# Performance work log

Measured on AMD Instinct MI355X. Metric: run time of the kernel, lower is better.

Reference implementation:

```python
import jax, jax.numpy as jnp
import numpy as np
from jax import lax

B, C, OUT, K, H, W = 8, 64, 32, 3, 64, 64


def _conv2d(x, w, b, stride=1, pad=0, groups=1):
    o = lax.conv_general_dilated(x, w, (stride, stride), [(pad, pad), (pad, pad)],
                                 dimension_numbers=('NCHW', 'OIHW', 'NCHW'),
                                 feature_group_count=groups)
    return o + b[None, :, None, None]


def _bn(x, g, b, m, v, eps=1e-5):
    # eval-mode BatchNorm2d with running stats
    s = g / jnp.sqrt(v + eps)
    return x * s[None, :, None, None] + (b - m * s)[None, :, None, None]


def _eca(x, w):
    # global avg pool -> 1D conv over channel axis -> sigmoid gate [b,c,1,1]
    y = x.mean((-2, -1))[:, None, :]  # [b,1,c]
    y = lax.conv_general_dilated(y, w, (1,), [(1, 1)],
                                 dimension_numbers=('NCW', 'OIW', 'NCW'))
    return jax.nn.sigmoid(y[:, 0, :])[:, :, None, None]


def _avgpool3(x):
    # AvgPool2d(k=3, stride=1, pad=1), count_include_pad=True (torch default)
    s = lax.reduce_window(x, 0.0, lax.add, (1, 1, 3, 3), (1, 1, 1, 1),
                          [(0, 0), (0, 0), (1, 1), (1, 1)])
    return s / 9.0


def _forward(x, sc_w, sc_b, ac_w, ac_b, oc_w, oc_b, oc_bn_g, oc_bn_b, oc_bn_m, oc_bn_v,
             ex_w, ey_w, ez_w, ff_w, ff_b, g1_w, g1_b, g2_w, g2_b,
             fu_w, fu_b, fu_bn_g, fu_bn_b, fu_bn_m, fu_bn_v):
    b, c, h, w = x.shape
    k = K
    # --- ReceptiveFieldAttentionConv ---
    frf = jax.nn.silu(_conv2d(x, sc_w, sc_b, pad=k // 2, groups=c))
    frf = frf.reshape(b, c, k * k, h, w)
    arf = _conv2d(_avgpool3(x), ac_w, ac_b, groups=c).reshape(b, c, k * k, h, w)
    arf = jax.nn.softmax(arf, axis=2)  # softmax over k*k RF positions
    wt = (frf * arf).reshape(b, c, k, k, h, w)
    wt = wt.transpose(0, 1, 4, 2, 5, 3).reshape(b, c, h * k, w * k)  # pixel-shuffle-like
    x_rfa = jax.nn.silu(_bn(_conv2d(wt, oc_w, oc_b, stride=k, groups=4),
                            oc_bn_g, oc_bn_b, oc_bn_m, oc_bn_v))
    # --- FrequencyGroupedChannelAttention ---
    energy = jnp.abs(jnp.fft.fft2(x)).mean((-2, -1))  # [b,c]
    ranks = jnp.argsort(jnp.argsort(-energy, axis=1), axis=1)
    mask = (ranks < c // 2).astype(x.dtype)[:, :, None, None]  # top-half-energy channels
    a_x = _eca(x, ex_w)
    a_y = _eca(x * mask, ey_w)
    a_z = _eca(x * (1.0 - mask), ez_w)
    a_f = _conv2d(jnp.concatenate([a_y, a_z], 1), ff_w, ff_b, groups=4)
    g_in = jnp.concatenate([a_f, a_x], 1)
    g = jax.nn.sigmoid(_conv2d(jax.nn.silu(_conv2d(g_in, g1_w, g1_b)), g2_w, g2_b))
    x_fgca = x * (g * a_f + (1.0 - g) * a_x)
    # --- fuse ---
    fused = jnp.concatenate([x_rfa, x_fgca], 1)
    return jax.nn.silu(_bn(_conv2d(fused, fu_w, fu_b),
                           fu_bn_g, fu_bn_b, fu_bn_m, fu_bn_v))


def setup_inputs() -> dict:
    key = jax.random.key(0)
    ks = jax.random.split(key, 32)
    rn = lambda k, shp, s=0.1: jax.random.normal(k, shp, jnp.float32) * s
    gh = max(8, C // 4)  # gate hidden = 16
    return {
        'x': jax.random.normal(ks[0], (B, C, H, W), jnp.float32),
        'sc_w': rn(ks[1], (C * K * K, 1, K, K)), 'sc_b': rn(ks[2], (C * K * K,)),
        'ac_w': rn(ks[3], (C * K * K, 1, 1, 1)), 'ac_b': rn(ks[4], (C * K * K,)),
        'oc_w': rn(ks[5], (C, C // 4, K, K)), 'oc_b': rn(ks[6], (C,)),
        'oc_bn_g': 1.0 + rn(ks[7], (C,)), 'oc_bn_b': rn(ks[8], (C,)),
        'oc_bn_m': rn(ks[9], (C,)), 'oc_bn_v': 0.9 + 0.2 * jax.random.uniform(ks[10], (C,), jnp.float32),
        'ex_w': rn(ks[11], (1, 1, 3), 0.3), 'ey_w': rn(ks[12], (1, 1, 3), 0.3),
        'ez_w': rn(ks[13], (1, 1, 3), 0.3),
        'ff_w': rn(ks[14], (C, 2 * C // 4, 1, 1)), 'ff_b': rn(ks[15], (C,)),
        'g1_w': rn(ks[16], (gh, 2 * C, 1, 1)), 'g1_b': rn(ks[17], (gh,)),
        'g2_w': rn(ks[18], (C, gh, 1, 1)), 'g2_b': rn(ks[19], (C,)),
        'fu_w': rn(ks[20], (OUT, 2 * C, 1, 1)), 'fu_b': rn(ks[21], (OUT,)),
        'fu_bn_g': 1.0 + rn(ks[22], (OUT,)), 'fu_bn_b': rn(ks[23], (OUT,)),
        'fu_bn_m': rn(ks[24], (OUT,)), 'fu_bn_v': 0.9 + 0.2 * jax.random.uniform(ks[25], (OUT,), jnp.float32),
    }


def reference(x, sc_w, sc_b, ac_w, ac_b, oc_w, oc_b, oc_bn_g, oc_bn_b, oc_bn_m, oc_bn_v,
              ex_w, ey_w, ez_w, ff_w, ff_b, g1_w, g1_b, g2_w, g2_b,
              fu_w, fu_b, fu_bn_g, fu_bn_b, fu_bn_m, fu_bn_v):
    return _forward(x, sc_w, sc_b, ac_w, ac_b, oc_w, oc_b, oc_bn_g, oc_bn_b, oc_bn_m, oc_bn_v,
                    ex_w, ey_w, ez_w, ff_w, ff_b, g1_w, g1_b, g2_w, g2_b,
                    fu_w, fu_b, fu_bn_g, fu_bn_b, fu_bn_m, fu_bn_v)
```

## Files before the change

kernel.cpp:

```cpp
#include <hip/hip_runtime.h>
#include <math.h>

#define EPS 1e-5f

__device__ __forceinline__ float wave_sum(float v) {
  v += __shfl_down(v, 32);
  v += __shfl_down(v, 16);
  v += __shfl_down(v, 8);
  v += __shfl_down(v, 4);
  v += __shfl_down(v, 2);
  v += __shfl_down(v, 1);
  return v;
}

__device__ __forceinline__ float silu_f(float v) { return v / (1.f + __expf(-v)); }
__device__ __forceinline__ float sigm_f(float v) { return 1.f / (1.f + __expf(-v)); }

__device__ __forceinline__ int bitrev6(int v) {
  return ((v & 1) << 5) | ((v & 2) << 3) | ((v & 4) << 1) |
         ((v & 8) >> 1) | ((v & 16) >> 3) | ((v & 32) >> 5);
}

__global__ __launch_bounds__(256) void k_dft(const float* __restrict__ x,
                                             float* __restrict__ energy,
                                             float* __restrict__ meanx) {
  __shared__ float re1[64 * 65];
  __shared__ float im1[64 * 65];
  __shared__ float redA[4], redB[4];
  const int bc = blockIdx.x;
  const int tid = threadIdx.x;
  const int lane = tid & 63;
  const int wv = tid >> 6;
  const float* xp = x + (size_t)bc * 4096;

  float twc[6], tws[6];
#pragma unroll
  for (int s = 0; s < 6; ++s) {
    int half = 32 >> s;
    if (lane & half) {
      float ang = -6.283185307179586f * (float)((lane & (half - 1)) << s) / 64.f;
      float sv, cv;
      __sincosf(ang, &sv, &cv);
      twc[s] = cv;
      tws[s] = sv;
    } else {
      twc[s] = 1.f;
      tws[s] = 0.f;
    }
  }

  const int f = bitrev6(lane);
  const int fm = (64 - f) & 63;
  const int plane = bitrev6(fm);

  float lsum = 0.f;
#pragma unroll 1
  for (int rp = 0; rp < 8; ++rp) {
    const int h0 = wv * 16 + rp * 2;
    float zr = xp[h0 * 64 + lane];
    float zi = xp[(h0 + 1) * 64 + lane];
    lsum += zr + zi;
#pragma unroll
    for (int s = 0; s < 6; ++s) {
      const int half = 32 >> s;
      const bool up = (lane & half) != 0;
      float pr = __shfl_xor(zr, half);
      float pi = __shfl_xor(zi, half);
      float tr = up ? pr - zr : zr + pr;
      float ti = up ? pi - zi : zi + pi;
      const float c = twc[s], sn = tws[s];
      zr = tr * c - ti * sn;
      zi = tr * sn + ti * c;
    }
    float mr = __shfl(zr, plane);
    float mi = __shfl(zi, plane);
    float ar = 0.5f * (zr + mr), ai = 0.5f * (zi - mi);
    float br = 0.5f * (zi + mi), bi = 0.5f * (mr - zr);
    re1[f * 65 + h0] = ar;
    im1[f * 65 + h0] = ai;
    re1[f * 65 + h0 + 1] = br;
    im1[f * 65 + h0 + 1] = bi;
  }
  __syncthreads();

  float msum = 0.f;
#pragma unroll 1
  for (int i = 0; i < 9; ++i) {
    const int kv = wv + 4 * i;
    if (kv > 32) break;
    const float wgt = (kv == 0 || kv == 32) ? 1.f : 2.f;
    float ar = re1[kv * 65 + lane];
    float ai = im1[kv * 65 + lane];
#pragma unroll
    for (int s = 0; s < 6; ++s) {
      const int half = 32 >> s;
      const bool up = (lane & half) != 0;
      float pr = __shfl_xor(ar, half);
      float pi = __shfl_xor(ai, half);
      float tr = up ? pr - ar : ar + pr;
      float ti = up ? pi - ai : ai + pi;
      const float c = twc[s], sn = tws[s];
      ar = tr * c - ti * sn;
      ai = tr * sn + ti * c;
    }
    msum += wgt * sqrtf(ar * ar + ai * ai);
  }

  msum = wave_sum(msum);
  lsum = wave_sum(lsum);
  if (lane == 0) { redA[wv] = msum; redB[wv] = lsum; }
  __syncthreads();
  if (tid == 0) {
    float e = redA[0] + redA[1] + redA[2] + redA[3];
    float m = redB[0] + redB[1] + redB[2] + redB[3];
    energy[bc] = e * (1.f / 4096.f);
    meanx[bc] = m * (1.f / 4096.f);
  }
}

__global__ __launch_bounds__(64) void k_attn(
    const float* __restrict__ energy, const float* __restrict__ meanx,
    const float* __restrict__ ex_w, const float* __restrict__ ey_w,
    const float* __restrict__ ez_w, const float* __restrict__ ff_w,
    const float* __restrict__ ff_b, const float* __restrict__ g1_w,
    const float* __restrict__ g1_b, const float* __restrict__ g2_w,
    const float* __restrict__ g2_b, float* __restrict__ s2) {
  __shared__ float e[64], mx[64], my[64], mz[64];
  __shared__ float ax[64], ay[64], az[64], af[64], h1[16];
  const int b = blockIdx.x;
  const int c = threadIdx.x;
  e[c] = energy[b * 64 + c];
  mx[c] = meanx[b * 64 + c];
  __syncthreads();
  int rank = 0;
  float ec = e[c];
  for (int i = 0; i < 64; ++i) {
    float ei = e[i];
    rank += (ei > ec) || (ei == ec && i < c);
  }
  float mask = (rank < 32) ? 1.f : 0.f;
  my[c] = mx[c] * mask;
  mz[c] = mx[c] * (1.f - mask);
  __syncthreads();
  {
    float l, r, m;
    l = (c > 0) ? mx[c - 1] : 0.f; m = mx[c]; r = (c < 63) ? mx[c + 1] : 0.f;
    ax[c] = sigm_f(ex_w[0] * l + ex_w[1] * m + ex_w[2] * r);
    l = (c > 0) ? my[c - 1] : 0.f; m = my[c]; r = (c < 63) ? my[c + 1] : 0.f;
    ay[c] = sigm_f(ey_w[0] * l + ey_w[1] * m + ey_w[2] * r);
    l = (c > 0) ? mz[c - 1] : 0.f; m = mz[c]; r = (c < 63) ? mz[c + 1] : 0.f;
    az[c] = sigm_f(ez_w[0] * l + ez_w[1] * m + ez_w[2] * r);
  }
  __syncthreads();
  {
    int g = c >> 4;
    float acc = ff_b[c];
#pragma unroll
    for (int i = 0; i < 32; ++i) {
      int ch = g * 32 + i;
      float v = (ch < 64) ? ay[ch] : az[ch - 64];
      acc = fmaf(v, ff_w[c * 32 + i], acc);
    }
    af[c] = acc;
  }
  __syncthreads();
  if (c < 16) {
    float a = g1_b[c];
#pragma unroll
    for (int i = 0; i < 64; ++i) a = fmaf(af[i], g1_w[c * 128 + i], a);
#pragma unroll
    for (int i = 0; i < 64; ++i) a = fmaf(ax[i], g1_w[c * 128 + 64 + i], a);
    h1[c] = silu_f(a);
  }
  __syncthreads();
  float gv = g2_b[c];
#pragma unroll
  for (int o = 0; o < 16; ++o) gv = fmaf(h1[o], g2_w[c * 16 + o], gv);
  gv = sigm_f(gv);
  s2[b * 64 + c] = gv * af[c] + (1.f - gv) * ax[c];
}

__global__ __launch_bounds__(256) void k_rfa(
    const float* __restrict__ x,
    const float* __restrict__ sc_w, const float* __restrict__ sc_b,
    const float* __restrict__ ac_w, const float* __restrict__ ac_b,
    const float* __restrict__ oc_w, const float* __restrict__ oc_b,
    const float* __restrict__ bn_g, const float* __restrict__ bn_b,
    const float* __restrict__ bn_m, const float* __restrict__ bn_v,
    float* __restrict__ xrfa) {
  __shared__ __align__(16) float scwp[16 * 9 * 12];
  __shared__ __align__(16) float mp[16 * 24];
  __shared__ __align__(16) float ocwp[16 * 16 * 12];
  const int blk = blockIdx.x;
  const int band = blk & 7;
  const int g = (blk >> 3) & 3;
  const int b = blk >> 5;
  const int tid = threadIdx.x;
  const int lane = tid & 63;
  const int wv = tid >> 6;

  for (int i = tid; i < 1296; i += 256) {
    int icg = i / 81, rem = i - icg * 81;
    int j = rem / 9, t = rem - j * 9;
    scwp[icg * 108 + j * 12 + t] = sc_w[(g * 144 + icg * 9 + j) * 9 + t];
  }
  if (tid < 144) {
    int icg = tid / 9, j = tid - icg * 9;
    scwp[icg * 108 + j * 12 + 9] = sc_b[g * 144 + tid];
    mp[icg * 24 + j] = ac_w[g * 144 + tid];
    mp[icg * 24 + 12 + j] = ac_b[g * 144 + tid];
  }
  for (int i = tid; i < 2304; i += 256) {
    int oco = i / 144, rem = i - oco * 144;
    int icg = rem / 9, j = rem - icg * 9;
    ocwp[icg * 192 + oco * 12 + j] = oc_w[((g * 16 + oco) * 16 + icg) * 9 + j];
  }
  __syncthreads();

  const int r0 = band * 8 + wv * 2;
  const int w = lane;
  const bool vW = w > 0, vE = w < 63;
  float acc0[16], acc1[16];
#pragma unroll
  for (int i = 0; i < 16; ++i) { acc0[i] = 0.f; acc1[i] = 0.f; }

  const float* xg = x + ((size_t)(b * 64 + g * 16)) * 4096 + w;

#pragma unroll 1
  for (int icg = 0; icg < 16; ++icg) {
    const float* xc = xg + icg * 4096;
    float n[12];
#pragma unroll
    for (int t = 0; t < 4; ++t) {
      int h = r0 - 1 + t;
      bool vh = (h >= 0) && (h < 64);
      const float* row = xc + h * 64;
      n[t * 3 + 0] = (vh && vW) ? row[-1] : 0.f;
      n[t * 3 + 1] = vh ? row[0] : 0.f;
      n[t * 3 + 2] = (vh && vE) ? row[1] : 0.f;
    }
    float rs0 = n[0] + n[1] + n[2];
    float rs1 = n[3] + n[4] + n[5];
    float rs2 = n[6] + n[7] + n[8];
    float rs3 = n[9] + n[10] + n[11];
    float ap0 = (rs0 + rs1 + rs2) * (1.f / 9.f);
    float ap1 = (rs1 + rs2 + rs3) * (1.f / 9.f);

    float aw[12], ab[12];
    *(float4*)&aw[0] = *(const float4*)&mp[icg * 24];
    *(float4*)&aw[4] = *(const float4*)&mp[icg * 24 + 4];
    *(float4*)&aw[8] = *(const float4*)&mp[icg * 24 + 8];
    *(float4*)&ab[0] = *(const float4*)&mp[icg * 24 + 12];
    *(float4*)&ab[4] = *(const float4*)&mp[icg * 24 + 16];
    *(float4*)&ab[8] = *(const float4*)&mp[icg * 24 + 20];

    float f0[9], f1[9], a0[9], a1[9];
    float amax0 = -1e30f, amax1 = -1e30f;
#pragma unroll
    for (int j = 0; j < 9; ++j) {
      float wt[12];
      *(float4*)&wt[0] = *(const float4*)&scwp[icg * 108 + j * 12];
      *(float4*)&wt[4] = *(const float4*)&scwp[icg * 108 + j * 12 + 4];
      *(float4*)&wt[8] = *(const float4*)&scwp[icg * 108 + j * 12 + 8];
      float p0 = wt[9], p1 = wt[9];
#pragma unroll
      for (int t = 0; t < 9; ++t) {
        p0 = fmaf(n[t], wt[t], p0);
        p1 = fmaf(n[t + 3], wt[t], p1);
      }
      f0[j] = silu_f(p0);
      f1[j] = silu_f(p1);
      float v0 = fmaf(ap0, aw[j], ab[j]);
      float v1 = fmaf(ap1, aw[j], ab[j]);
      a0[j] = v0; a1[j] = v1;
      amax0 = fmaxf(amax0, v0);
      amax1 = fmaxf(amax1, v1);
    }
    float es0 = 0.f, es1 = 0.f;
    float p0[9], p1[9];
#pragma unroll
    for (int j = 0; j < 9; ++j) {
      float e0 = __expf(a0[j] - amax0);
      float e1 = __expf(a1[j] - amax1);
      es0 += e0; es1 += e1;
      p0[j] = f0[j] * e0;
      p1[j] = f1[j] * e1;
    }
    float i0 = __fdividef(1.f, es0);
    float i1 = __fdividef(1.f, es1);
#pragma unroll
    for (int j = 0; j < 9; ++j) { p0[j] *= i0; p1[j] *= i1; }

#pragma unroll
    for (int oco = 0; oco < 16; ++oco) {
      float ov[12];
      *(float4*)&ov[0] = *(const float4*)&ocwp[icg * 192 + oco * 12];
      *(float4*)&ov[4] = *(const float4*)&ocwp[icg * 192 + oco * 12 + 4];
      *(float4*)&ov[8] = *(const float4*)&ocwp[icg * 192 + oco * 12 + 8];
      float s0 = 0.f, s1 = 0.f;
#pragma unroll
      for (int j = 0; j < 9; ++j) {
        s0 = fmaf(p0[j], ov[j], s0);
        s1 = fmaf(p1[j], ov[j], s1);
      }
      acc0[oco] += s0;
      acc1[oco] += s1;
    }
  }

  float* op = xrfa + ((size_t)(b * 64 + g * 16)) * 4096 + r0 * 64 + w;
#pragma unroll
  for (int oco = 0; oco < 16; ++oco) {
    int oc = g * 16 + oco;
    float s = bn_g[oc] * rsqrtf(bn_v[oc] + EPS);
    float bb = bn_b[oc] - bn_m[oc] * s;
    float ob = oc_b[oc];
    float v0 = fmaf(acc0[oco] + ob, s, bb);
    float v1 = fmaf(acc1[oco] + ob, s, bb);
    op[oco * 4096] = silu_f(v0);
    op[oco * 4096 + 64] = silu_f(v1);
  }
}

__global__ __launch_bounds__(256) void k_fuse(
    const float* __restrict__ x, const float* __restrict__ xrfa,
    const float* __restrict__ s2, const float* __restrict__ fu_w,
    const float* __restrict__ fu_b, const float* __restrict__ bn_g,
    const float* __restrict__ bn_b, const float* __restrict__ bn_m,
    const float* __restrict__ bn_v, float* __restrict__ out) {
  __shared__ float red[3 * 64 * 33];
  __shared__ __align__(16) float fw[4096];
  const int blk = blockIdx.x;
  const int tid = threadIdx.x;
  const int sloc = tid & 63;
  const int chunk = __builtin_amdgcn_readfirstlane(tid >> 6);
  const int b = blk >> 6;
  const int sp = (blk & 63) * 64 + sloc;
  const int cb = (chunk & 1) * 32;
  const int wb = chunk * 32;

  for (int i = tid; i < 1024; i += 256)
    ((float4*)fw)[i] = ((const float4*)fu_w)[i];

  const float* src = (chunk < 2) ? xrfa : x;
  const float* ip = src + ((size_t)(b * 64 + cb)) * 4096 + sp;
  float inv[32];
  if (chunk < 2) {
#pragma unroll
    for (int i = 0; i < 32; ++i) inv[i] = ip[i * 4096];
  } else {
#pragma unroll
    for (int i = 0; i < 32; ++i) inv[i] = ip[i * 4096] * s2[b * 64 + cb + i];
  }
  __syncthreads();

  float acc[32];
#pragma unroll
  for (int oc = 0; oc < 32; ++oc) {
    const float* wr = &fw[oc * 128 + wb];
    float a = 0.f;
#pragma unroll
    for (int q = 0; q < 8; ++q) {
      float4 wv4 = *(const float4*)&wr[q * 4];
      a = fmaf(inv[q * 4 + 0], wv4.x, a);
      a = fmaf(inv[q * 4 + 1], wv4.y, a);
      a = fmaf(inv[q * 4 + 2], wv4.z, a);
      a = fmaf(inv[q * 4 + 3], wv4.w, a);
    }
    acc[oc] = a;
  }

  if (chunk != 0) {
    float* rp = &red[(chunk - 1) * 2112 + sloc * 33];
#pragma unroll
    for (int oc = 0; oc < 32; ++oc) rp[oc] = acc[oc];
  }
  __syncthreads();
  if (chunk == 0) {
#pragma unroll
    for (int oc = 0; oc < 32; ++oc)
      acc[oc] += red[sloc * 33 + oc] + red[2112 + sloc * 33 + oc] +
                 red[4224 + sloc * 33 + oc];
    float* op = out + ((size_t)b * 32) * 4096 + sp;
#pragma unroll
    for (int oc = 0; oc < 32; ++oc) {
      float s = bn_g[oc] * rsqrtf(bn_v[oc] + EPS);
      float v = acc[oc] + fu_b[oc];
      v = fmaf(v, s, bn_b[oc] - bn_m[oc] * s);
      op[oc * 4096] = silu_f(v);
    }
  }
}

extern "C" void kernel_launch(void* const* d_in, const int* in_sizes, int n_in,
                              void* d_out, int out_size, void* d_ws, size_t ws_size,
                              hipStream_t stream) {
  const float* x       = (const float*)d_in[0];
  const float* sc_w    = (const float*)d_in[1];
  const float* sc_b    = (const float*)d_in[2];
  const float* ac_w    = (const float*)d_in[3];
  const float* ac_b    = (const float*)d_in[4];
  const float* oc_w    = (const float*)d_in[5];
  const float* oc_b    = (const float*)d_in[6];
  const float* oc_bn_g = (const float*)d_in[7];
  const float* oc_bn_b = (const float*)d_in[8];
  const float* oc_bn_m = (const float*)d_in[9];
  const float* oc_bn_v = (const float*)d_in[10];
  const float* ex_w    = (const float*)d_in[11];
  const float* ey_w    = (const float*)d_in[12];
  const float* ez_w    = (const float*)d_in[13];
  const float* ff_w    = (const float*)d_in[14];
  const float* ff_b    = (const float*)d_in[15];
  const float* g1_w    = (const float*)d_in[16];
  const float* g1_b    = (const float*)d_in[17];
  const float* g2_w    = (const float*)d_in[18];
  const float* g2_b    = (const float*)d_in[19];
  const float* fu_w    = (const float*)d_in[20];
  const float* fu_b    = (const float*)d_in[21];
  const float* fu_bn_g = (const float*)d_in[22];
  const float* fu_bn_b = (const float*)d_in[23];
  const float* fu_bn_m = (const float*)d_in[24];
  const float* fu_bn_v = (const float*)d_in[25];

  float* ws     = (float*)d_ws;
  float* energy = ws;
  float* meanx  = ws + 512;
  float* s2     = ws + 1024;
  float* xrfa   = ws + 2048;

  k_dft<<<512, 256, 0, stream>>>(x, energy, meanx);
  k_attn<<<8, 64, 0, stream>>>(energy, meanx, ex_w, ey_w, ez_w,
                               ff_w, ff_b, g1_w, g1_b, g2_w, g2_b, s2);
  k_rfa<<<256, 256, 0, stream>>>(x, sc_w, sc_b, ac_w, ac_b, oc_w, oc_b,
                                 oc_bn_g, oc_bn_b, oc_bn_m, oc_bn_v, xrfa);
  k_fuse<<<512, 256, 0, stream>>>(x, xrfa, s2, fu_w, fu_b,
                                  fu_bn_g, fu_bn_b, fu_bn_m, fu_bn_v,
                                  (float*)d_out);
}
```

Baseline: 190.3 us.

## Batch FFT rows, split RFA channel loop across waves, reorganize fuse by output channel

Three kernels change together. The DFT kernel now handles two complex row pairs per butterfly pass, keeps only the non-redundant half spectrum (f<=32) in shared memory, and transforms two columns per iteration. The RFA conv kernel doubles its grid by splitting the 16 input channels between wave pairs and summing the partials through shared memory. The fuse kernel makes each wave load all 128 input channels and compute 8 output channels, which removes the cross-wave reduction. Together these aim to raise parallelism and ILP and cut shared-memory and reduction overhead, at the cost of higher register pressure in the fuse kernel (128 live inputs) and an extra shared-memory reduction step in RFA.

```diff
diff --git a/kernel.cpp b/kernel.cpp
--- a/kernel.cpp
+++ b/kernel.cpp
@@ -21,11 +21,26 @@
          ((v & 8) >> 1) | ((v & 16) >> 3) | ((v & 32) >> 5);
 }
 
+#define FFT6(zr, zi)                                           \
+  do {                                                         \
+    _Pragma("unroll") for (int s = 0; s < 6; ++s) {            \
+      const int half = 32 >> s;                                \
+      const bool up = (lane & half) != 0;                      \
+      float pr = __shfl_xor(zr, half);                         \
+      float pi = __shfl_xor(zi, half);                         \
+      float tr = up ? pr - zr : zr + pr;                       \
+      float ti = up ? pi - zi : zi + pi;                       \
+      const float c = twc[s], sn = tws[s];                     \
+      zr = tr * c - ti * sn;                                   \
+      zi = tr * sn + ti * c;                                   \
+    }                                                          \
+  } while (0)
+
 __global__ __launch_bounds__(256) void k_dft(const float* __restrict__ x,
                                              float* __restrict__ energy,
                                              float* __restrict__ meanx) {
-  __shared__ float re1[64 * 65];
-  __shared__ float im1[64 * 65];
+  __shared__ float re1[33 * 65];
+  __shared__ float im1[33 * 65];
   __shared__ float redA[4], redB[4];
   const int bc = blockIdx.x;
   const int tid = threadIdx.x;
@@ -55,55 +70,82 @@
 
   float lsum = 0.f;
 #pragma unroll 1
-  for (int rp = 0; rp < 8; ++rp) {
-    const int h0 = wv * 16 + rp * 2;
-    float zr = xp[h0 * 64 + lane];
-    float zi = xp[(h0 + 1) * 64 + lane];
-    lsum += zr + zi;
+  for (int rp = 0; rp < 4; ++rp) {
+    const int h0 = wv * 16 + rp * 4;
+    float x0 = xp[h0 * 64 + lane];
+    float x1 = xp[(h0 + 1) * 64 + lane];
+    float x2 = xp[(h0 + 2) * 64 + lane];
+    float x3 = xp[(h0 + 3) * 64 + lane];
+    lsum += x0 + x1 + x2 + x3;
+    float zr = x0, zi = x1, yr = x2, yi = x3;
 #pragma unroll
     for (int s = 0; s < 6; ++s) {
       const int half = 32 >> s;
       const bool up = (lane & half) != 0;
-      float pr = __shfl_xor(zr, half);
-      float pi = __shfl_xor(zi, half);
-      float tr = up ? pr - zr : zr + pr;
-      float ti = up ? pi - zi : zi + pi;
+      float pzr = __shfl_xor(zr, half);
+      float pzi = __shfl_xor(zi, half);
+      float pyr = __shfl_xor(yr, half);
+      float pyi = __shfl_xor(yi, half);
+      float tzr = up ? pzr - zr : zr + pzr;
+      float tzi = up ? pzi - zi : zi + pzi;
+      float tyr = up ? pyr - yr : yr + pyr;
+      float tyi = up ? pyi - yi : yi + pyi;
       const float c = twc[s], sn = tws[s];
-      zr = tr * c - ti * sn;
-      zi = tr * sn + ti * c;
-    }
-    float mr = __shfl(zr, plane);
-    float mi = __shfl(zi, plane);
-    float ar = 0.5f * (zr + mr), ai = 0.5f * (zi - mi);
-    float br = 0.5f * (zi + mi), bi = 0.5f * (mr - zr);
-    re1[f * 65 + h0] = ar;
-    im1[f * 65 + h0] = ai;
-    re1[f * 65 + h0 + 1] = br;
-    im1[f * 65 + h0 + 1] = bi;
+      zr = tzr * c - tzi * sn;
+      zi = tzr * sn + tzi * c;
+      yr = tyr * c - tyi * sn;
+      yi = tyr * sn + tyi * c;
+    }
+    float mzr = __shfl(zr, plane), mzi = __shfl(zi, plane);
+    float myr = __shfl(yr, plane), myi = __shfl(yi, plane);
+    if (f <= 32) {
+      float ar = 0.5f * (zr + mzr), ai = 0.5f * (zi - mzi);
+      float br = 0.5f * (zi + mzi), bi = 0.5f * (mzr - zr);
+      float cr = 0.5f * (yr + myr), ci = 0.5f * (yi - myi);
+      float dr = 0.5f * (yi + myi), di = 0.5f * (myr - yr);
+      re1[f * 65 + h0] = ar;     im1[f * 65 + h0] = ai;
+      re1[f * 65 + h0 + 1] = br; im1[f * 65 + h0 + 1] = bi;
+      re1[f * 65 + h0 + 2] = cr; im1[f * 65 + h0 + 2] = ci;
+      re1[f * 65 + h0 + 3] = dr; im1[f * 65 + h0 + 3] = di;
+    }
   }
   __syncthreads();
 
   float msum = 0.f;
 #pragma unroll 1
-  for (int i = 0; i < 9; ++i) {
-    const int kv = wv + 4 * i;
-    if (kv > 32) break;
-    const float wgt = (kv == 0 || kv == 32) ? 1.f : 2.f;
-    float ar = re1[kv * 65 + lane];
-    float ai = im1[kv * 65 + lane];
+  for (int i = 0; i < 4; ++i) {
+    const int kv1 = wv + 8 * i;
+    const int kv2 = kv1 + 4;
+    const float w1 = (kv1 == 0) ? 1.f : 2.f;
+    float ar = re1[kv1 * 65 + lane];
+    float ai = im1[kv1 * 65 + lane];
+    float br = re1[kv2 * 65 + lane];
+    float bi = im1[kv2 * 65 + lane];
 #pragma unroll
     for (int s = 0; s < 6; ++s) {
       const int half = 32 >> s;
       const bool up = (lane & half) != 0;
-      float pr = __shfl_xor(ar, half);
-      float pi = __shfl_xor(ai, half);
-      float tr = up ? pr - ar : ar + pr;
-      float ti = up ? pi - ai : ai + pi;
+      float par = __shfl_xor(ar, half);
+      float pai = __shfl_xor(ai, half);
+      float pbr = __shfl_xor(br, half);
+      float pbi = __shfl_xor(bi, half);
+      float tar = up ? par - ar : ar + par;
+      float tai = up ? pai - ai : ai + pai;
+      float tbr = up ? pbr - br : br + pbr;
+      float tbi = up ? pbi - bi : bi + pbi;
       const float c = twc[s], sn = tws[s];
-      ar = tr * c - ti * sn;
-      ai = tr * sn + ti * c;
-    }
-    msum += wgt * sqrtf(ar * ar + ai * ai);
+      ar = tar * c - tai * sn;
+      ai = tar * sn + tai * c;
+      br = tbr * c - tbi * sn;
+      bi = tbr * sn + tbi * c;
+    }
+    msum += w1 * sqrtf(ar * ar + ai * ai) + 2.f * sqrtf(br * br + bi * bi);
+  }
+  if (wv == 0) {
+    float ar = re1[32 * 65 + lane];
+    float ai = im1[32 * 65 + lane];
+    FFT6(ar, ai);
+    msum += sqrtf(ar * ar + ai * ai);
   }
 
   msum = wave_sum(msum);
@@ -191,13 +233,16 @@
   __shared__ __align__(16) float scwp[16 * 9 * 12];
   __shared__ __align__(16) float mp[16 * 24];
   __shared__ __align__(16) float ocwp[16 * 16 * 12];
+  __shared__ float red[128 * 33];
   const int blk = blockIdx.x;
-  const int band = blk & 7;
-  const int g = (blk >> 3) & 3;
-  const int b = blk >> 5;
+  const int band = blk & 15;
+  const int g = (blk >> 4) & 3;
+  const int b = blk >> 6;
   const int tid = threadIdx.x;
   const int lane = tid & 63;
   const int wv = tid >> 6;
+  const int wp = wv & 1;
+  const int half = wv >> 1;
 
   for (int i = tid; i < 1296; i += 256) {
     int icg = i / 81, rem = i - icg * 81;
@@ -217,7 +262,7 @@
   }
   __syncthreads();
 
-  const int r0 = band * 8 + wv * 2;
+  const int r0 = band * 4 + wp * 2;
   const int w = lane;
   const bool vW = w > 0, vE = w < 63;
   float acc0[16], acc1[16];
@@ -225,9 +270,11 @@
   for (int i = 0; i < 16; ++i) { acc0[i] = 0.f; acc1[i] = 0.f; }
 
   const float* xg = x + ((size_t)(b * 64 + g * 16)) * 4096 + w;
+  const int icg0 = half * 8;
 
 #pragma unroll 1
-  for (int icg = 0; icg < 16; ++icg) {
+  for (int ii = 0; ii < 8; ++ii) {
+    const int icg = icg0 + ii;
     const float* xc = xg + icg * 4096;
     float n[12];
 #pragma unroll
@@ -308,17 +355,33 @@
     }
   }
 
-  float* op = xrfa + ((size_t)(b * 64 + g * 16)) * 4096 + r0 * 64 + w;
-#pragma unroll
-  for (int oco = 0; oco < 16; ++oco) {
-    int oc = g * 16 + oco;
-    float s = bn_g[oc] * rsqrtf(bn_v[oc] + EPS);
-    float bb = bn_b[oc] - bn_m[oc] * s;
-    float ob = oc_b[oc];
-    float v0 = fmaf(acc0[oco] + ob, s, bb);
-    float v1 = fmaf(acc1[oco] + ob, s, bb);
-    op[oco * 4096] = silu_f(v0);
-    op[oco * 4096 + 64] = silu_f(v1);
+  const int rid = wp * 64 + lane;
+  if (half == 1) {
+#pragma unroll
+    for (int k = 0; k < 16; ++k) {
+      red[rid * 33 + k] = acc0[k];
+      red[rid * 33 + 16 + k] = acc1[k];
+    }
+  }
+  __syncthreads();
+  if (half == 0) {
+#pragma unroll
+    for (int k = 0; k < 16; ++k) {
+      acc0[k] += red[rid * 33 + k];
+      acc1[k] += red[rid * 33 + 16 + k];
+    }
+    float* op = xrfa + ((size_t)(b * 64 + g * 16)) * 4096 + r0 * 64 + w;
+#pragma unroll
+    for (int oco = 0; oco < 16; ++oco) {
+      int oc = g * 16 + oco;
+      float s = bn_g[oc] * rsqrtf(bn_v[oc] + EPS);
+      float bb = bn_b[oc] - bn_m[oc] * s;
+      float ob = oc_b[oc];
+      float v0 = fmaf(acc0[oco] + ob, s, bb);
+      float v1 = fmaf(acc1[oco] + ob, s, bb);
+      op[oco * 4096] = silu_f(v0);
+      op[oco * 4096 + 64] = silu_f(v1);
+    }
   }
 }
 
@@ -328,67 +391,56 @@
     const float* __restrict__ fu_b, const float* __restrict__ bn_g,
     const float* __restrict__ bn_b, const float* __restrict__ bn_m,
     const float* __restrict__ bn_v, float* __restrict__ out) {
-  __shared__ float red[3 * 64 * 33];
   __shared__ __align__(16) float fw[4096];
+  __shared__ float s2l[64];
   const int blk = blockIdx.x;
   const int tid = threadIdx.x;
   const int sloc = tid & 63;
-  const int chunk = __builtin_amdgcn_readfirstlane(tid >> 6);
+  const int ocq = tid >> 6;
   const int b = blk >> 6;
   const int sp = (blk & 63) * 64 + sloc;
-  const int cb = (chunk & 1) * 32;
-  const int wb = chunk * 32;
 
   for (int i = tid; i < 1024; i += 256)
     ((float4*)fw)[i] = ((const float4*)fu_w)[i];
-
-  const float* src = (chunk < 2) ? xrfa : x;
-  const float* ip = src + ((size_t)(b * 64 + cb)) * 4096 + sp;
-  float inv[32];
-  if (chunk < 2) {
-#pragma unroll
-    for (int i = 0; i < 32; ++i) inv[i] = ip[i * 4096];
-  } else {
-#pragma unroll
-    for (int i = 0; i < 32; ++i) inv[i] = ip[i * 4096] * s2[b * 64 + cb + i];
-  }
-  __syncthreads();
-
-  float acc[32];
-#pragma unroll
-  for (int oc = 0; oc < 32; ++oc) {
-    const float* wr = &fw[oc * 128 + wb];
+  if (tid < 64) s2l[tid] = s2[b * 64 + tid];
+
+  const float* xr = xrfa + (size_t)b * 64 * 4096 + sp;
+  const float* xp = x + (size_t)b * 64 * 4096 + sp;
+  float va[64], vb[64];
+#pragma unroll
+  for (int i = 0; i < 64; ++i) va[i] = xr[i * 4096];
+#pragma unroll
+  for (int i = 0; i < 64; ++i) vb[i] = xp[i * 4096];
+  __syncthreads();
+#pragma unroll
+  for (int i = 0; i < 64; ++i) vb[i] *= s2l[i];
+
+  float* op = out + (size_t)b * 32 * 4096 + sp;
+#pragma unroll 1
+  for (int o = 0; o < 8; ++o) {
+    const int oc = ocq * 8 + o;
+    const float* wr = &fw[oc * 128];
     float a = 0.f;
 #pragma unroll
-    for (int q = 0; q < 8; ++q) {
-      float4 wv4 = *(const float4*)&wr[q * 4];
-      a = fmaf(inv[q * 4 + 0], wv4.x, a);
-      a = fmaf(inv[q * 4 + 1], wv4.y, a);
-      a = fmaf(inv[q * 4 + 2], wv4.z, a);
-      a = fmaf(inv[q * 4 + 3], wv4.w, a);
-    }
-    acc[oc] = a;
-  }
-
-  if (chunk != 0) {
-    float* rp = &red[(chunk - 1) * 2112 + sloc * 33];
-#pragma unroll
-    for (int oc = 0; oc < 32; ++oc) rp[oc] = acc[oc];
-  }
-  __syncthreads();
-  if (chunk == 0) {
-#pragma unroll
-    for (int oc = 0; oc < 32; ++oc)
-      acc[oc] += red[sloc * 33 + oc] + red[2112 + sloc * 33 + oc] +
-                 red[4224 + sloc * 33 + oc];
-    float* op = out + ((size_t)b * 32) * 4096 + sp;
-#pragma unroll
-    for (int oc = 0; oc < 32; ++oc) {
-      float s = bn_g[oc] * rsqrtf(bn_v[oc] + EPS);
-      float v = acc[oc] + fu_b[oc];
-      v = fmaf(v, s, bn_b[oc] - bn_m[oc] * s);
-      op[oc * 4096] = silu_f(v);
-    }
+    for (int q = 0; q < 16; ++q) {
+      float4 w4 = *(const float4*)&wr[q * 4];
+      a = fmaf(va[q * 4 + 0], w4.x, a);
+      a = fmaf(va[q * 4 + 1], w4.y, a);
+      a = fmaf(va[q * 4 + 2], w4.z, a);
+      a = fmaf(va[q * 4 + 3], w4.w, a);
+    }
+#pragma unroll
+    for (int q = 0; q < 16; ++q) {
+      float4 w4 = *(const float4*)&wr[64 + q * 4];
+      a = fmaf(vb[q * 4 + 0], w4.x, a);
+      a = fmaf(vb[q * 4 + 1], w4.y, a);
+      a = fmaf(vb[q * 4 + 2], w4.z, a);
+      a = fmaf(vb[q * 4 + 3], w4.w, a);
+    }
+    float s = bn_g[oc] * rsqrtf(bn_v[oc] + EPS);
+    float v = a + fu_b[oc];
+    v = fmaf(v, s, bn_b[oc] - bn_m[oc] * s);
+    op[oc * 4096] = silu_f(v);
   }
 }
 
@@ -431,7 +483,7 @@
   k_dft<<<512, 256, 0, stream>>>(x, energy, meanx);
   k_attn<<<8, 64, 0, stream>>>(energy, meanx, ex_w, ey_w, ez_w,
                                ff_w, ff_b, g1_w, g1_b, g2_w, g2_b, s2);
-  k_rfa<<<256, 256, 0, stream>>>(x, sc_w, sc_b, ac_w, ac_b, oc_w, oc_b,
+  k_rfa<<<512, 256, 0, stream>>>(x, sc_w, sc_b, ac_w, ac_b, oc_w, oc_b,
                                  oc_bn_g, oc_bn_b, oc_bn_m, oc_bn_v, xrfa);
   k_fuse<<<512, 256, 0, stream>>>(x, xrfa, s2, fu_w, fu_b,
                                   fu_bn_g, fu_bn_b, fu_bn_m, fu_bn_v,
```

New measurement: 174.1 us. 1.09x faster.
